# Performance work log

Measured on AMD Instinct MI355X. Metric: run time of the kernel, lower is better.

Reference implementation:

```python
import jax, jax.numpy as jnp
import numpy as np

# MLA dims (DeepSeek-V2-Lite-class)
B, S, D = 2, 2048, 2048
H = 16
NOPE, ROPE, VD = 128, 64, 128   # qk_nope_head_dim, qk_rope_head_dim, v_head_dim
KV_RANK, Q_RANK = 512, 1536
EPS = 1e-6
THETA = 10000.0


def setup_inputs() -> dict:
    key = jax.random.key(0)
    ks = jax.random.split(key, 8)

    def init(k, shape, fan_in):
        return jax.random.normal(k, shape, jnp.float32) * (fan_in ** -0.5)

    return {
        "x": jax.random.normal(ks[0], (B, S, D), jnp.float32),
        "w_dq": init(ks[1], (D, Q_RANK), D),
        "q_a_norm": jnp.ones((Q_RANK,), jnp.float32),
        "w_uq": init(ks[2], (Q_RANK, H * (NOPE + ROPE)), Q_RANK),
        "w_dkv": init(ks[3], (D, KV_RANK + ROPE), D),
        "kv_a_norm": jnp.ones((KV_RANK,), jnp.float32),
        "w_ukv": init(ks[4], (KV_RANK, H * (NOPE + VD)), KV_RANK),
        "w_o": init(ks[5], (H * VD, D), H * VD),
    }


def _rmsnorm(x, w):
    return x * jax.lax.rsqrt(jnp.mean(x * x, axis=-1, keepdims=True) + EPS) * w


def _rope(x):
    # x: [B, S, H', d] -> rotary on last dim (half-split style)
    d = x.shape[-1]
    inv = 1.0 / (THETA ** (jnp.arange(0, d, 2, dtype=jnp.float32) / d))
    ang = jnp.arange(x.shape[1], dtype=jnp.float32)[:, None] * inv[None, :]  # [S, d/2]
    cos = jnp.cos(ang)[None, :, None, :]
    sin = jnp.sin(ang)[None, :, None, :]
    x1, x2 = jnp.split(x, 2, axis=-1)
    return jnp.concatenate([x1 * cos - x2 * sin, x2 * cos + x1 * sin], axis=-1)


def reference(x, w_dq, q_a_norm, w_uq, w_dkv, kv_a_norm, w_ukv, w_o):
    # --- low-rank Q projection ---
    q = _rmsnorm(x @ w_dq, q_a_norm) @ w_uq          # [B,S,H*(NOPE+ROPE)]
    q = q.reshape(B, S, H, NOPE + ROPE)
    q_nope, q_pe = q[..., :NOPE], q[..., NOPE:]

    # --- latent (compressed) KV projection + shared decoupled-RoPE key ---
    ckv = x @ w_dkv                                   # [B,S,KV_RANK+ROPE]
    c_kv, k_pe = ckv[..., :KV_RANK], ckv[..., KV_RANK:]
    kv = (_rmsnorm(c_kv, kv_a_norm) @ w_ukv).reshape(B, S, H, NOPE + VD)
    k_nope, v = kv[..., :NOPE], kv[..., NOPE:]

    # --- decoupled RoPE on rope dims only ---
    q_pe = _rope(q_pe)                                # [B,S,H,ROPE]
    k_pe = _rope(k_pe[:, :, None, :])                 # [B,S,1,ROPE] shared across heads

    qf = jnp.concatenate([q_nope, q_pe], axis=-1)     # [B,S,H,NOPE+ROPE]
    kf = jnp.concatenate([k_nope, jnp.broadcast_to(k_pe, (B, S, H, ROPE))], axis=-1)

    # --- scaled dot-product attention with causal mask ---
    scale = 1.0 / jnp.sqrt(jnp.float32(NOPE + ROPE))
    scores = jnp.einsum("bqhd,bkhd->bhqk", qf * scale, kf)  # [B,H,S,S]
    causal = jnp.tril(jnp.ones((S, S), bool))
    scores = jnp.where(causal[None, None], scores, -1e9)
    w = jax.nn.softmax(scores, axis=-1)
    o = jnp.einsum("bhqk,bkhd->bqhd", w, v).reshape(B, S, H * VD)
    return o @ w_o                                    # [B,S,D]
```

## Files before the change

### kernel.cpp

```cpp
#include <hip/hip_runtime.h>
#include <hip/hip_bf16.h>
#include <math.h>

#define SS 2048
#define HH 16
#define EPSF 1e-6f
#define MR 4096
#define L2T 13.287712379549449f
#define ASCL (0.07216878364870322f * 1.4426950408889634f)

typedef unsigned short u16;
typedef unsigned int u32;
typedef __attribute__((ext_vector_type(8))) short bf8_t;
typedef __attribute__((ext_vector_type(4))) float f4_t;

__device__ inline u16 f2b(float f) {
    __hip_bfloat16 h = __float2bfloat16(f);
    return __builtin_bit_cast(u16, h);
}
__device__ inline float b2f(u16 x) {
    u32 v = (u32)x << 16;
    return __builtin_bit_cast(float, v);
}

#define GLD16(g, l) __builtin_amdgcn_global_load_lds( \
    (const __attribute__((address_space(1))) u32*)(g), \
    (__attribute__((address_space(3))) u32*)(l), 16, 0, 0)

#define MFMA16(a,b,c) __builtin_amdgcn_mfma_f32_16x16x32_bf16((a),(b),(c),0,0,0)

__global__ void prep_k(const float* __restrict__ x, u16* __restrict__ xb,
                       const float* __restrict__ w_dq, const float* __restrict__ w_dkv,
                       const float* __restrict__ w_uq, const float* __restrict__ w_ukv,
                       const float* __restrict__ w_o,
                       u16* __restrict__ wT1, u16* __restrict__ wTuq,
                       u16* __restrict__ wTukv, u16* __restrict__ wTo) {
    __shared__ float tt[32][33];
    int blk = blockIdx.x, tid = threadIdx.x;
    if (blk < 8192) {
        int i = blk * 256 + tid;
        float4 v = ((const float4*)x)[i];
        ushort4 o;
        o.x = f2b(v.x); o.y = f2b(v.y); o.z = f2b(v.z); o.w = f2b(v.w);
        *(ushort4*)(xb + (size_t)i * 4) = o;
        return;
    }
    blk -= 8192;
    const float* W; u16* dst; int K, N, Npad, nx;
    if (blk < 3072)       { W = w_dq;  dst = wT1;                      K = 2048; N = 1536; Npad = 1536; nx = 48; }
    else if (blk < 4352)  { blk -= 3072; W = w_dkv; dst = wT1 + (size_t)1536 * 2048; K = 2048; N = 576;  Npad = 640;  nx = 20; }
    else if (blk < 8960)  { blk -= 4352; W = w_uq;  dst = wTuq;        K = 1536; N = 3072; Npad = 3072; nx = 96; }
    else if (blk < 11008) { blk -= 8960; W = w_ukv; dst = wTukv;       K = 512;  N = 4096; Npad = 4096; nx = 128; }
    else                  { blk -= 11008; W = w_o;  dst = wTo;         K = 2048; N = 2048; Npad = 2048; nx = 64; }
    int n0 = (blk % nx) * 32, k0 = (blk / nx) * 32;
    int tx = tid & 31, ty = tid >> 5;
    for (int i = ty; i < 32; i += 8) {
        int n = n0 + tx;
        tt[i][tx] = (n < N) ? W[(size_t)(k0 + i) * N + n] : 0.f;
    }
    __syncthreads();
    for (int i = ty; i < 32; i += 8) {
        int n = n0 + i;
        if (n < Npad) dst[(size_t)n * K + k0 + tx] = f2b(tt[tx][i]);
    }
}

template <int MODE, int MINW>
__global__ __launch_bounds__(256, MINW)
void gemm_mfma(const u16* __restrict__ A, const u16* __restrict__ BT,
               void* __restrict__ Cv, void* __restrict__ Cv2, int K, int N) {
    __shared__ u16 lA[128 * 32];
    __shared__ u16 lB[128 * 32];
    const int tid = threadIdx.x;
    const int w = tid >> 6, lane = tid & 63;
    const int quad = lane >> 4, col = lane & 15;
    const int wm = (w >> 1) * 64, wn = (w & 1) * 64;
    const int bm = blockIdx.y * 128, bn = blockIdx.x * 128;
    const int srow = lane >> 2;
    const int scol = (lane & 3) * 8;
    f4_t acc[4][4] = {};
    for (int k0 = 0; k0 < K; k0 += 32) {
        __syncthreads();
        #pragma unroll
        for (int cc = 0; cc < 2; cc++) {
            int c = 2 * w + cc;
            int row = c * 16 + srow;
            GLD16(A  + (size_t)(bm + row) * K + k0 + scol, (char*)lA + c * 1024);
            GLD16(BT + (size_t)(bn + row) * K + k0 + scol, (char*)lB + c * 1024);
        }
        __syncthreads();
        bf8_t af[4], bf[4];
        #pragma unroll
        for (int i = 0; i < 4; i++) {
            af[i] = *(const bf8_t*)(lA + (wm + i * 16 + col) * 32 + quad * 8);
            bf[i] = *(const bf8_t*)(lB + (wn + i * 16 + col) * 32 + quad * 8);
        }
        #pragma unroll
        for (int mi = 0; mi < 4; mi++)
            #pragma unroll
            for (int ni = 0; ni < 4; ni++)
                acc[mi][ni] = MFMA16(af[mi], bf[ni], acc[mi][ni]);
    }
    if (MODE == 0) {
        float* C = (float*)Cv;
        #pragma unroll
        for (int mi = 0; mi < 4; mi++)
            #pragma unroll
            for (int ni = 0; ni < 4; ni++) {
                int n = bn + wn + ni * 16 + col;
                #pragma unroll
                for (int r = 0; r < 4; r++) {
                    int m = bm + wm + mi * 16 + quad * 4 + r;
                    C[(size_t)m * N + n] = acc[mi][ni][r];
                }
            }
    } else if (MODE == 1) {
        u16* C = (u16*)Cv;
        #pragma unroll
        for (int mi = 0; mi < 4; mi++)
            #pragma unroll
            for (int ni = 0; ni < 4; ni++) {
                int n = bn + wn + ni * 16 + col;
                #pragma unroll
                for (int r = 0; r < 4; r++) {
                    int m = bm + wm + mi * 16 + quad * 4 + r;
                    C[(size_t)m * N + n] = f2b(acc[mi][ni][r]);
                }
            }
    } else if (MODE == 2) {
        u16* C = (u16*)Cv;
        int span = ((bn + wn) >> 6) % 3;
        if (span < 2) {
            #pragma unroll
            for (int mi = 0; mi < 4; mi++)
                #pragma unroll
                for (int ni = 0; ni < 4; ni++) {
                    int n = bn + wn + ni * 16 + col;
                    #pragma unroll
                    for (int r = 0; r < 4; r++) {
                        int m = bm + wm + mi * 16 + quad * 4 + r;
                        C[(size_t)m * N + n] = f2b(acc[mi][ni][r] * ASCL);
                    }
                }
        } else {
            #pragma unroll
            for (int ni = 0; ni < 2; ni++) {
                int e = ni * 16 + col;
                float inv = exp2f(-(float)e * (L2T / 32.0f));
                #pragma unroll
                for (int mi = 0; mi < 4; mi++) {
                    #pragma unroll
                    for (int r = 0; r < 4; r++) {
                        int m = bm + wm + mi * 16 + quad * 4 + r;
                        int pos = m & (SS - 1);
                        float ang = (float)pos * inv;
                        float cs, sn; sincosf(ang, &sn, &cs);
                        float x1 = acc[mi][ni][r], x2 = acc[mi][ni + 2][r];
                        int n = bn + wn + ni * 16 + col;
                        C[(size_t)m * N + n]      = f2b((x1 * cs - x2 * sn) * ASCL);
                        C[(size_t)m * N + n + 32] = f2b((x2 * cs + x1 * sn) * ASCL);
                    }
                }
            }
        }
    } else {
        u16* kb = (u16*)Cv;
        u16* vT = (u16*)Cv2;
        #pragma unroll
        for (int ni = 0; ni < 4; ni++) {
            int nb = bn + wn + ni * 16;
            int h = nb >> 8;
            int cb = nb & 255;
            if (cb < 128) {
                #pragma unroll
                for (int mi = 0; mi < 4; mi++)
                    #pragma unroll
                    for (int r = 0; r < 4; r++) {
                        int m = bm + wm + mi * 16 + quad * 4 + r;
                        kb[((size_t)m * HH + h) * 192 + cb + col] = f2b(acc[mi][ni][r]);
                    }
            } else {
                int dv = cb - 128 + col;
                #pragma unroll
                for (int mi = 0; mi < 4; mi++) {
                    int mb = bm + wm + mi * 16 + quad * 4;
                    ushort4 o;
                    o.x = f2b(acc[mi][ni][0]);
                    o.y = f2b(acc[mi][ni][1]);
                    o.z = f2b(acc[mi][ni][2]);
                    o.w = f2b(acc[mi][ni][3]);
                    *(ushort4*)(vT + ((size_t)h * 128 + dv) * 4096 + mb) = o;
                }
            }
        }
    }
}

__global__ void rms_all_k(const u16* __restrict__ C1, const float* __restrict__ wq,
                          const float* __restrict__ wkv,
                          u16* __restrict__ qlb, u16* __restrict__ ckvnb,
                          u16* __restrict__ kb) {
    __shared__ float red[256];
    int tid = threadIdx.x;
    if (blockIdx.x < 4096) {
        int row = blockIdx.x;
        const ushort4* rp = (const ushort4*)(C1 + (size_t)row * 2176);
        float s = 0.f;
        for (int i = tid; i < 384; i += 256) {
            ushort4 u = rp[i];
            float a = b2f(u.x), b = b2f(u.y), c = b2f(u.z), d = b2f(u.w);
            s += a * a + b * b + c * c + d * d;
        }
        red[tid] = s;
        __syncthreads();
        for (int off = 128; off > 0; off >>= 1) {
            if (tid < off) red[tid] += red[tid + off];
            __syncthreads();
        }
        float sc = rsqrtf(red[0] * (1.0f / 1536.0f) + EPSF);
        ushort4* op = (ushort4*)(qlb + (size_t)row * 1536);
        const float4* wv = (const float4*)wq;
        for (int i = tid; i < 384; i += 256) {
            ushort4 u = rp[i];
            float4 ww = wv[i];
            ushort4 o;
            o.x = f2b(b2f(u.x) * sc * ww.x);
            o.y = f2b(b2f(u.y) * sc * ww.y);
            o.z = f2b(b2f(u.z) * sc * ww.z);
            o.w = f2b(b2f(u.w) * sc * ww.w);
            op[i] = o;
        }
    } else {
        int row = blockIdx.x - 4096;
        const u16* base = C1 + (size_t)row * 2176 + 1536;
        if (tid < 32) {
            int t = tid;
            float x1 = b2f(base[512 + t]), x2 = b2f(base[544 + t]);
            int pos = row & (SS - 1);
            float inv = exp2f(-(float)t * (L2T / 32.0f));
            float ang = (float)pos * inv;
            float cs, sn; sincosf(ang, &sn, &cs);
            u16 y1 = f2b(x1 * cs - x2 * sn);
            u16 y2 = f2b(x2 * cs + x1 * sn);
            u16* kr = kb + (size_t)row * HH * 192;
            #pragma unroll
            for (int h = 0; h < HH; h++) {
                kr[h * 192 + 128 + t] = y1;
                kr[h * 192 + 160 + t] = y2;
            }
        }
        const ushort4* rp = (const ushort4*)base;
        float s = 0.f;
        if (tid < 128) {
            ushort4 u = rp[tid];
            float a = b2f(u.x), b = b2f(u.y), c = b2f(u.z), d = b2f(u.w);
            s = a * a + b * b + c * c + d * d;
        }
        red[tid] = s;
        __syncthreads();
        for (int off = 128; off > 0; off >>= 1) {
            if (tid < off) red[tid] += red[tid + off];
            __syncthreads();
        }
        float sc = rsqrtf(red[0] * (1.0f / 512.0f) + EPSF);
        if (tid < 128) {
            ushort4 u = rp[tid];
            float4 ww = ((const float4*)wkv)[tid];
            ushort4 o;
            o.x = f2b(b2f(u.x) * sc * ww.x);
            o.y = f2b(b2f(u.y) * sc * ww.y);
            o.z = f2b(b2f(u.z) * sc * ww.z);
            o.w = f2b(b2f(u.w) * sc * ww.w);
            ((ushort4*)(ckvnb + (size_t)row * 512))[tid] = o;
        }
    }
}

__global__ __launch_bounds__(256, 2)
void attn_mfma(const u16* __restrict__ qb, const u16* __restrict__ kb,
               const u16* __restrict__ vT, u16* __restrict__ ob) {
    __shared__ u16 lK[2][64 * 200];
    __shared__ u16 lP[4 * 16 * 72];
    const int tid = threadIdx.x, w = tid >> 6, lane = tid & 63;
    const int quad = lane >> 4, col = lane & 15;
    const int bh = blockIdx.x, b = bh >> 4, h = bh & 15;
    const int tok0 = b * SS;
    int goff[7];
    #pragma unroll
    for (int jj = 0; jj < 7; jj++) {
        int c = w + 4 * jj;
        int o_b = c * 1024 + lane * 16;
        int row = o_b / 400;
        int ro = o_b - row * 400;
        goff[jj] = (ro < 384) ? (row * HH + h) * 192 + (ro >> 1) : 0;
    }
    u16* pw = lP + w * 16 * 72;

    for (int ph = 0; ph < 2; ph++) {
        const int qt = ph ? (31 - (int)blockIdx.y) : (int)blockIdx.y;
        bf8_t qf[6];
        {
            int qtok = tok0 + qt * 64 + w * 16 + col;
            const u16* qp = qb + ((size_t)qtok * HH + h) * 192 + quad * 8;
            #pragma unroll
            for (int kc = 0; kc < 6; kc++) qf[kc] = *(const bf8_t*)(qp + kc * 32);
        }
        f4_t o[8] = {};
        float mrow[4] = {-1e30f, -1e30f, -1e30f, -1e30f};
        float lrow[4] = {0.f, 0.f, 0.f, 0.f};
        {
            size_t kbase = (size_t)(tok0) * (HH * 192);
            #pragma unroll
            for (int jj = 0; jj < 7; jj++) {
                int c = w + 4 * jj;
                if (c < 25) GLD16(kb + kbase + goff[jj], (char*)lK[0] + c * 1024);
            }
        }
        __syncthreads();
        for (int kt = 0; kt <= qt; kt++) {
            const u16* cur = lK[kt & 1];
            if (kt < qt) {
                size_t kbase = (size_t)(tok0 + (kt + 1) * 64) * (HH * 192);
                u16* nxt = (u16*)lK[(kt + 1) & 1];
                #pragma unroll
                for (int jj = 0; jj < 7; jj++) {
                    int c = w + 4 * jj;
                    if (c < 25) GLD16(kb + kbase + goff[jj], (char*)nxt + c * 1024);
                }
            }
            bf8_t vf[2][8];
            {
                const u16* vbase = vT + (size_t)(h * 128 + col) * 4096
                                 + tok0 + kt * 64 + quad * 8;
                #pragma unroll
                for (int kc2 = 0; kc2 < 2; kc2++)
                    #pragma unroll
                    for (int n = 0; n < 8; n++)
                        vf[kc2][n] = *(const bf8_t*)(vbase + (size_t)(n * 16) * 4096 + kc2 * 32);
            }
            bool diag = (kt == qt);
            f4_t s[4] = {};
            #pragma unroll
            for (int t = 0; t < 4; t++) {
                if (!diag || t <= w) {
                    #pragma unroll
                    for (int kc = 0; kc < 6; kc++) {
                        bf8_t kf = *(const bf8_t*)(cur + (t * 16 + col) * 200 + kc * 32 + quad * 8);
                        s[t] = MFMA16(qf[kc], kf, s[t]);
                    }
                }
            }
            if (diag) {
                #pragma unroll
                for (int t = 0; t < 4; t++) {
                    int kg = t * 16 + col;
                    #pragma unroll
                    for (int r = 0; r < 4; r++) {
                        int qg = w * 16 + quad * 4 + r;
                        if (kg > qg) s[t][r] = -1e30f;
                    }
                }
            }
            float sm[4] = {-1e30f, -1e30f, -1e30f, -1e30f};
            #pragma unroll
            for (int t = 0; t < 4; t++)
                #pragma unroll
                for (int r = 0; r < 4; r++) sm[r] = fmaxf(sm[r], s[t][r]);
            #pragma unroll
            for (int off = 1; off < 16; off <<= 1)
                #pragma unroll
                for (int r = 0; r < 4; r++) sm[r] = fmaxf(sm[r], __shfl_xor(sm[r], off));
            float al[4];
            #pragma unroll
            for (int r = 0; r < 4; r++) {
                float mn = fmaxf(mrow[r], sm[r]);
                al[r] = exp2f(mrow[r] - mn);
                mrow[r] = mn;
            }
            float rs[4] = {0.f, 0.f, 0.f, 0.f};
            #pragma unroll
            for (int t = 0; t < 4; t++)
                #pragma unroll
                for (int r = 0; r < 4; r++) {
                    float p = exp2f(s[t][r] - mrow[r]);
                    s[t][r] = p;
                    rs[r] += p;
                }
            #pragma unroll
            for (int off = 1; off < 16; off <<= 1)
                #pragma unroll
                for (int r = 0; r < 4; r++) rs[r] += __shfl_xor(rs[r], off);
            #pragma unroll
            for (int r = 0; r < 4; r++) lrow[r] = lrow[r] * al[r] + rs[r];
            #pragma unroll
            for (int n = 0; n < 8; n++)
                #pragma unroll
                for (int r = 0; r < 4; r++) o[n][r] *= al[r];
            #pragma unroll
            for (int t = 0; t < 4; t++)
                #pragma unroll
                for (int r = 0; r < 4; r++)
                    pw[(quad * 4 + r) * 72 + t * 16 + col] = f2b(s[t][r]);
            #pragma unroll
            for (int kc2 = 0; kc2 < 2; kc2++) {
                bf8_t pf = *(const bf8_t*)(pw + col * 72 + kc2 * 32 + quad * 8);
                #pragma unroll
                for (int n = 0; n < 8; n++)
                    o[n] = MFMA16(pf, vf[kc2][n], o[n]);
            }
            __syncthreads();
        }
        #pragma unroll
        for (int n = 0; n < 8; n++)
            #pragma unroll
            for (int r = 0; r < 4; r++) {
                int qtok = tok0 + qt * 64 + w * 16 + quad * 4 + r;
                ob[((size_t)qtok * HH + h) * 128 + n * 16 + col] = f2b(o[n][r] / lrow[r]);
            }
    }
}

extern "C" void kernel_launch(void* const* d_in, const int* in_sizes, int n_in,
                              void* d_out, int out_size, void* d_ws, size_t ws_size,
                              hipStream_t stream) {
    const float* x        = (const float*)d_in[0];
    const float* w_dq     = (const float*)d_in[1];
    const float* q_a_norm = (const float*)d_in[2];
    const float* w_uq     = (const float*)d_in[3];
    const float* w_dkv    = (const float*)d_in[4];
    const float* kv_a_nrm = (const float*)d_in[5];
    const float* w_ukv    = (const float*)d_in[6];
    const float* w_o      = (const float*)d_in[7];
    float* out = (float*)d_out;

    char* ws = (char*)d_ws;
    const size_t MB = 1024 * 1024;
    u16* xb    = (u16*)(ws);
    u16* wT1   = (u16*)(ws + 17 * MB);
    u16* wTuq  = (u16*)(ws + 26 * MB);
    u16* wTukv = (u16*)(ws + 36 * MB);
    u16* wTo   = (u16*)(ws + 41 * MB);
    u16* C1    = (u16*)(ws + 50 * MB);
    u16* qlb   = (u16*)(ws + 68 * MB);
    u16* qbuf  = (u16*)(ws + 81 * MB);
    u16* ckvnb = (u16*)(ws + 107 * MB);
    u16* kb    = (u16*)(ws + 112 * MB);
    u16* vT    = (u16*)(ws + 138 * MB);
    u16* aob   = xb;

    prep_k<<<23296, 256, 0, stream>>>(x, xb, w_dq, w_dkv, w_uq, w_ukv, w_o,
                                      wT1, wTuq, wTukv, wTo);
    gemm_mfma<1, 3><<<dim3(17, 32), 256, 0, stream>>>(xb, wT1, C1, nullptr, 2048, 2176);
    rms_all_k<<<8192, 256, 0, stream>>>(C1, q_a_norm, kv_a_nrm, qlb, ckvnb, kb);
    gemm_mfma<2, 2><<<dim3(24, 32), 256, 0, stream>>>(qlb, wTuq, qbuf, nullptr, 1536, 3072);
    gemm_mfma<3, 3><<<dim3(32, 32), 256, 0, stream>>>(ckvnb, wTukv, kb, vT, 512, 4096);
    attn_mfma<<<dim3(32, 16), 256, 0, stream>>>(qbuf, kb, vT, aob);
    gemm_mfma<0, 3><<<dim3(16, 32), 256, 0, stream>>>(aob, wTo, out, nullptr, 2048, 2048);
}
```

Baseline: 498.1 us.

## Stage V tiles in LDS, drop K double-buffering, one q-tile per block

The attention kernel now loads both K and V tiles into shared memory with async global-to-LDS copies, instead of reading V fragments straight from global memory in each wave. K goes from double-buffered to single-buffered, which cuts LDS use so launch bounds can rise to 3 blocks per CU. Each block now handles one query tile instead of a balanced pair, so the grid doubles to 32x32. The trade-off is losing load/compute overlap (two syncs per iteration, no prefetch) and losing causal load balancing across blocks, in exchange for more occupancy and shared V reuse across the four waves.

```diff
diff --git a/kernel.cpp b/kernel.cpp
--- a/kernel.cpp
+++ b/kernel.cpp
@@ -276,148 +276,134 @@
     }
 }
 
-__global__ __launch_bounds__(256, 2)
+__global__ __launch_bounds__(256, 3)
 void attn_mfma(const u16* __restrict__ qb, const u16* __restrict__ kb,
                const u16* __restrict__ vT, u16* __restrict__ ob) {
-    __shared__ u16 lK[2][64 * 200];
+    __shared__ u16 lK[64 * 200];
+    __shared__ u16 lV[128 * 72];
     __shared__ u16 lP[4 * 16 * 72];
     const int tid = threadIdx.x, w = tid >> 6, lane = tid & 63;
     const int quad = lane >> 4, col = lane & 15;
     const int bh = blockIdx.x, b = bh >> 4, h = bh & 15;
+    const int qt = 31 - (int)blockIdx.y;
     const int tok0 = b * SS;
-    int goff[7];
+    int goff[11];
     #pragma unroll
-    for (int jj = 0; jj < 7; jj++) {
+    for (int jj = 0; jj < 11; jj++) {
         int c = w + 4 * jj;
-        int o_b = c * 1024 + lane * 16;
-        int row = o_b / 400;
-        int ro = o_b - row * 400;
-        goff[jj] = (ro < 384) ? (row * HH + h) * 192 + (ro >> 1) : 0;
+        if (c < 25) {
+            int o = c * 1024 + lane * 16;
+            int row = o / 400, ro = o - row * 400;
+            goff[jj] = (ro < 384) ? (row * HH + h) * 192 + (ro >> 1) : 0;
+        } else {
+            int c2 = c - 25;
+            int o = c2 * 1024 + lane * 16;
+            int row = o / 144, ro = o - row * 144;
+            goff[jj] = (ro < 128) ? (h * 128 + row) * 4096 + (ro >> 1) : 0;
+        }
     }
     u16* pw = lP + w * 16 * 72;
-
-    for (int ph = 0; ph < 2; ph++) {
-        const int qt = ph ? (31 - (int)blockIdx.y) : (int)blockIdx.y;
-        bf8_t qf[6];
-        {
-            int qtok = tok0 + qt * 64 + w * 16 + col;
-            const u16* qp = qb + ((size_t)qtok * HH + h) * 192 + quad * 8;
-            #pragma unroll
-            for (int kc = 0; kc < 6; kc++) qf[kc] = *(const bf8_t*)(qp + kc * 32);
-        }
-        f4_t o[8] = {};
-        float mrow[4] = {-1e30f, -1e30f, -1e30f, -1e30f};
-        float lrow[4] = {0.f, 0.f, 0.f, 0.f};
-        {
-            size_t kbase = (size_t)(tok0) * (HH * 192);
-            #pragma unroll
-            for (int jj = 0; jj < 7; jj++) {
-                int c = w + 4 * jj;
-                if (c < 25) GLD16(kb + kbase + goff[jj], (char*)lK[0] + c * 1024);
-            }
-        }
-        __syncthreads();
-        for (int kt = 0; kt <= qt; kt++) {
-            const u16* cur = lK[kt & 1];
-            if (kt < qt) {
-                size_t kbase = (size_t)(tok0 + (kt + 1) * 64) * (HH * 192);
-                u16* nxt = (u16*)lK[(kt + 1) & 1];
-                #pragma unroll
-                for (int jj = 0; jj < 7; jj++) {
-                    int c = w + 4 * jj;
-                    if (c < 25) GLD16(kb + kbase + goff[jj], (char*)nxt + c * 1024);
-                }
-            }
-            bf8_t vf[2][8];
-            {
-                const u16* vbase = vT + (size_t)(h * 128 + col) * 4096
-                                 + tok0 + kt * 64 + quad * 8;
-                #pragma unroll
-                for (int kc2 = 0; kc2 < 2; kc2++)
-                    #pragma unroll
-                    for (int n = 0; n < 8; n++)
-                        vf[kc2][n] = *(const bf8_t*)(vbase + (size_t)(n * 16) * 4096 + kc2 * 32);
-            }
-            bool diag = (kt == qt);
-            f4_t s[4] = {};
+    bf8_t qf[6];
+    {
+        int qtok = tok0 + qt * 64 + w * 16 + col;
+        const u16* qp = qb + ((size_t)qtok * HH + h) * 192 + quad * 8;
+        #pragma unroll
+        for (int kc = 0; kc < 6; kc++) qf[kc] = *(const bf8_t*)(qp + kc * 32);
+    }
+    f4_t o[8] = {};
+    float mrow[4] = {-1e30f, -1e30f, -1e30f, -1e30f};
+    float lrow[4] = {0.f, 0.f, 0.f, 0.f};
+    for (int kt = 0; kt <= qt; kt++) {
+        size_t kbase = (size_t)(tok0 + kt * 64) * (HH * 192);
+        size_t vbase = (size_t)(tok0 + kt * 64);
+        __syncthreads();
+        #pragma unroll
+        for (int jj = 0; jj < 11; jj++) {
+            int c = w + 4 * jj;
+            if (c < 25)      GLD16(kb + kbase + goff[jj], (char*)lK + c * 1024);
+            else if (c < 43) GLD16(vT + vbase + goff[jj], (char*)lV + (c - 25) * 1024);
+        }
+        __syncthreads();
+        bool diag = (kt == qt);
+        f4_t s[4] = {};
+        #pragma unroll
+        for (int t = 0; t < 4; t++) {
+            if (!diag || t <= w) {
+                #pragma unroll
+                for (int kc = 0; kc < 6; kc++) {
+                    bf8_t kf = *(const bf8_t*)(lK + (t * 16 + col) * 200 + kc * 32 + quad * 8);
+                    s[t] = MFMA16(qf[kc], kf, s[t]);
+                }
+            }
+        }
+        if (diag) {
             #pragma unroll
             for (int t = 0; t < 4; t++) {
-                if (!diag || t <= w) {
-                    #pragma unroll
-                    for (int kc = 0; kc < 6; kc++) {
-                        bf8_t kf = *(const bf8_t*)(cur + (t * 16 + col) * 200 + kc * 32 + quad * 8);
-                        s[t] = MFMA16(qf[kc], kf, s[t]);
-                    }
-                }
-            }
-            if (diag) {
-                #pragma unroll
-                for (int t = 0; t < 4; t++) {
-                    int kg = t * 16 + col;
-                    #pragma unroll
-                    for (int r = 0; r < 4; r++) {
-                        int qg = w * 16 + quad * 4 + r;
-                        if (kg > qg) s[t][r] = -1e30f;
-                    }
-                }
-            }
-            float sm[4] = {-1e30f, -1e30f, -1e30f, -1e30f};
-            #pragma unroll
-            for (int t = 0; t < 4; t++)
-                #pragma unroll
-                for (int r = 0; r < 4; r++) sm[r] = fmaxf(sm[r], s[t][r]);
-            #pragma unroll
-            for (int off = 1; off < 16; off <<= 1)
-                #pragma unroll
-                for (int r = 0; r < 4; r++) sm[r] = fmaxf(sm[r], __shfl_xor(sm[r], off));
-            float al[4];
+                int kg = t * 16 + col;
+                #pragma unroll
+                for (int r = 0; r < 4; r++) {
+                    int qg = w * 16 + quad * 4 + r;
+                    if (kg > qg) s[t][r] = -1e30f;
+                }
+            }
+        }
+        float sm[4] = {-1e30f, -1e30f, -1e30f, -1e30f};
+        #pragma unroll
+        for (int t = 0; t < 4; t++)
+            #pragma unroll
+            for (int r = 0; r < 4; r++) sm[r] = fmaxf(sm[r], s[t][r]);
+        #pragma unroll
+        for (int off = 1; off < 16; off <<= 1)
+            #pragma unroll
+            for (int r = 0; r < 4; r++) sm[r] = fmaxf(sm[r], __shfl_xor(sm[r], off));
+        float al[4];
+        #pragma unroll
+        for (int r = 0; r < 4; r++) {
+            float mn = fmaxf(mrow[r], sm[r]);
+            al[r] = exp2f(mrow[r] - mn);
+            mrow[r] = mn;
+        }
+        float rs[4] = {0.f, 0.f, 0.f, 0.f};
+        #pragma unroll
+        for (int t = 0; t < 4; t++)
             #pragma unroll
             for (int r = 0; r < 4; r++) {
-                float mn = fmaxf(mrow[r], sm[r]);
-                al[r] = exp2f(mrow[r] - mn);
-                mrow[r] = mn;
-            }
-            float rs[4] = {0.f, 0.f, 0.f, 0.f};
-            #pragma unroll
-            for (int t = 0; t < 4; t++)
-                #pragma unroll
-                for (int r = 0; r < 4; r++) {
-                    float p = exp2f(s[t][r] - mrow[r]);
-                    s[t][r] = p;
-                    rs[r] += p;
-                }
-            #pragma unroll
-            for (int off = 1; off < 16; off <<= 1)
-                #pragma unroll
-                for (int r = 0; r < 4; r++) rs[r] += __shfl_xor(rs[r], off);
-            #pragma unroll
-            for (int r = 0; r < 4; r++) lrow[r] = lrow[r] * al[r] + rs[r];
-            #pragma unroll
-            for (int n = 0; n < 8; n++)
-                #pragma unroll
-                for (int r = 0; r < 4; r++) o[n][r] *= al[r];
-            #pragma unroll
-            for (int t = 0; t < 4; t++)
-                #pragma unroll
-                for (int r = 0; r < 4; r++)
-                    pw[(quad * 4 + r) * 72 + t * 16 + col] = f2b(s[t][r]);
-            #pragma unroll
-            for (int kc2 = 0; kc2 < 2; kc2++) {
-                bf8_t pf = *(const bf8_t*)(pw + col * 72 + kc2 * 32 + quad * 8);
-                #pragma unroll
-                for (int n = 0; n < 8; n++)
-                    o[n] = MFMA16(pf, vf[kc2][n], o[n]);
-            }
-            __syncthreads();
-        }
+                float p = exp2f(s[t][r] - mrow[r]);
+                s[t][r] = p;
+                rs[r] += p;
+            }
+        #pragma unroll
+        for (int off = 1; off < 16; off <<= 1)
+            #pragma unroll
+            for (int r = 0; r < 4; r++) rs[r] += __shfl_xor(rs[r], off);
+        #pragma unroll
+        for (int r = 0; r < 4; r++) lrow[r] = lrow[r] * al[r] + rs[r];
         #pragma unroll
         for (int n = 0; n < 8; n++)
             #pragma unroll
-            for (int r = 0; r < 4; r++) {
-                int qtok = tok0 + qt * 64 + w * 16 + quad * 4 + r;
-                ob[((size_t)qtok * HH + h) * 128 + n * 16 + col] = f2b(o[n][r] / lrow[r]);
-            }
-    }
+            for (int r = 0; r < 4; r++) o[n][r] *= al[r];
+        #pragma unroll
+        for (int t = 0; t < 4; t++)
+            #pragma unroll
+            for (int r = 0; r < 4; r++)
+                pw[(quad * 4 + r) * 72 + t * 16 + col] = f2b(s[t][r]);
+        #pragma unroll
+        for (int kc2 = 0; kc2 < 2; kc2++) {
+            bf8_t pf = *(const bf8_t*)(pw + col * 72 + kc2 * 32 + quad * 8);
+            #pragma unroll
+            for (int n = 0; n < 8; n++) {
+                bf8_t vf = *(const bf8_t*)(lV + (n * 16 + col) * 72 + kc2 * 32 + quad * 8);
+                o[n] = MFMA16(pf, vf, o[n]);
+            }
+        }
+    }
+    #pragma unroll
+    for (int n = 0; n < 8; n++)
+        #pragma unroll
+        for (int r = 0; r < 4; r++) {
+            int qtok = tok0 + qt * 64 + w * 16 + quad * 4 + r;
+            ob[((size_t)qtok * HH + h) * 128 + n * 16 + col] = f2b(o[n][r] / lrow[r]);
+        }
 }
 
 extern "C" void kernel_launch(void* const* d_in, const int* in_sizes, int n_in,
@@ -454,6 +440,6 @@
     rms_all_k<<<8192, 256, 0, stream>>>(C1, q_a_norm, kv_a_nrm, qlb, ckvnb, kb);
     gemm_mfma<2, 2><<<dim3(24, 32), 256, 0, stream>>>(qlb, wTuq, qbuf, nullptr, 1536, 3072);
     gemm_mfma<3, 3><<<dim3(32, 32), 256, 0, stream>>>(ckvnb, wTukv, kb, vT, 512, 4096);
-    attn_mfma<<<dim3(32, 16), 256, 0, stream>>>(qbuf, kb, vT, aob);
+    attn_mfma<<<dim3(32, 32), 256, 0, stream>>>(qbuf, kb, vT, aob);
     gemm_mfma<0, 3><<<dim3(16, 32), 256, 0, stream>>>(aob, wTo, out, nullptr, 2048, 2048);
 }
```

After: 452.3 us. -9.2%, faster.
